# Kernel optimization log

Measured on AMD Instinct MI355X. Metric: run time of the kernel, lower is better.

The kernel has to match this reference:

```python
import jax, jax.numpy as jnp
import numpy as np

B, S, D, H = 2, 2048, 1024, 16
HD = D // H
EPS = 1e-5


def layer_norm(x, g, b):
    m = jnp.mean(x, axis=-1, keepdims=True)
    v = jnp.mean(jnp.square(x - m), axis=-1, keepdims=True)
    return (x - m) * jax.lax.rsqrt(v + EPS) * g + b


def setup_inputs() -> dict:
    key = jax.random.key(0)
    ks = jax.random.split(key, 16)
    s = 0.02
    x = jax.random.normal(ks[0], (B, S, D), dtype=jnp.float32)
    mask = jax.random.randint(ks[1], (1, 1, S, S), 0, 2, dtype=jnp.int32)
    return {
        "x": x,
        "mask": mask,
        "Wq": jax.random.normal(ks[2], (D, D), jnp.float32) * s,
        "Wk": jax.random.normal(ks[3], (D, D), jnp.float32) * s,
        "Wv": jax.random.normal(ks[4], (D, D), jnp.float32) * s,
        "Wo": jax.random.normal(ks[5], (D, D), jnp.float32) * s,
        "bo": jax.random.normal(ks[6], (D,), jnp.float32) * s,
        "ln1_g": jnp.ones((D,), jnp.float32),
        "ln1_b": jnp.zeros((D,), jnp.float32),
        "W1": jax.random.normal(ks[7], (D, 4 * D), jnp.float32) * s,
        "b1": jax.random.normal(ks[8], (4 * D,), jnp.float32) * s,
        "W2": jax.random.normal(ks[9], (4 * D, D), jnp.float32) * s,
        "b2": jax.random.normal(ks[10], (D,), jnp.float32) * s,
        "ln2_g": jnp.ones((D,), jnp.float32),
        "ln2_b": jnp.zeros((D,), jnp.float32),
    }


def reference(x, mask, Wq, Wk, Wv, Wo, bo, ln1_g, ln1_b, W1, b1, W2, b2, ln2_g, ln2_b):
    # --- multi-head attention (dropout = identity in eval) ---
    q = (x @ Wq).reshape(B, S, H, HD)
    k = (x @ Wk).reshape(B, S, H, HD)
    v = (x @ Wv).reshape(B, S, H, HD)
    scores = jnp.einsum("bshd,bthd->bhst", q, k) / jnp.sqrt(jnp.float32(HD))
    scores = jnp.where(mask == 1, jnp.float32(-1e9), scores)
    p = jax.nn.softmax(scores, axis=-1)
    o = jnp.einsum("bhst,bthd->bshd", p, v).reshape(B, S, D)
    attn_out = o @ Wo + bo
    # --- residual with norm on the branch (note: norm applied to attn output) ---
    x = x + layer_norm(attn_out, ln1_g, ln1_b)
    # --- FFN: gelu after fc1 AND after fc2 (as in source) ---
    h = jax.nn.gelu(x @ W1 + b1, approximate=False)
    h = jax.nn.gelu(h @ W2 + b2, approximate=False)
    x = x + layer_norm(h, ln2_g, ln2_b)
    return x
```

## Files before the change

### kernel.cpp

```cpp
#include <hip/hip_runtime.h>
#include <hip/hip_bf16.h>
#include <cstdint>

#define BB 2
#define SS 2048
#define DD 1024
#define HH 16
#define HDIM 64
#define MROWS (BB*SS)

typedef __bf16 bf16;
using bf16x8 = __bf16 __attribute__((ext_vector_type(8)));
using bf16x4 = __bf16 __attribute__((ext_vector_type(4)));
using bf16x2 = __bf16 __attribute__((ext_vector_type(2)));
using f32x4  = float __attribute__((ext_vector_type(4)));

__device__ __forceinline__ float gelu_exact(float x) {
    return 0.5f * x * (1.f + erff(x * 0.70710678118654752f));
}

__device__ __forceinline__ void stage16(const bf16* g, bf16* lds_chunk_base, int lane) {
#if __has_builtin(__builtin_amdgcn_global_load_lds)
    __builtin_amdgcn_global_load_lds((const __attribute__((address_space(1))) void*)g,
                                     (__attribute__((address_space(3))) void*)lds_chunk_base,
                                     16, 0, 0);
#else
    *(bf16x8*)(lds_chunk_base + lane * 8) = *(const bf16x8*)g;
#endif
}

__global__ __launch_bounds__(256) void prep_kernel(
    const float* __restrict__ x, bf16* __restrict__ x_b,
    const int* __restrict__ mask, unsigned long long* __restrict__ maskb,
    const float* __restrict__ Wq, const float* __restrict__ Wk,
    const float* __restrict__ Wv, const float* __restrict__ Wo,
    const float* __restrict__ W1, const float* __restrict__ W2,
    bf16* __restrict__ Wqkv_t, bf16* __restrict__ Wo_t,
    bf16* __restrict__ W1_t, bf16* __restrict__ W2_t) {
    const int bid = blockIdx.x;
    if (bid < 4096) {
        int i = bid * 256 + threadIdx.x;
        float4 v = ((const float4*)x)[i];
        bf16x4 o;
        o[0] = (bf16)v.x; o[1] = (bf16)v.y; o[2] = (bf16)v.z; o[3] = (bf16)v.w;
        *(bf16x4*)(x_b + (size_t)i * 4) = o;
        return;
    }
    if (bid < 20480) {
        int gid = (bid - 4096) * 256 + threadIdx.x;
        int mv = mask[gid];
        unsigned long long bal = __ballot(mv == 1);
        if ((threadIdx.x & 63) == 0) maskb[gid >> 6] = bal;
        return;
    }
    int t = bid - 20480;
    const float* W; bf16* Wt; int K, N, bx, by;
    if (t < 4096) {
        int wsel = t >> 10;
        int tt = t & 1023;
        W  = (wsel == 0) ? Wq : (wsel == 1) ? Wk : (wsel == 2) ? Wv : Wo;
        Wt = (wsel == 3) ? Wo_t : (Wqkv_t + (size_t)wsel * 1024 * 1024);
        K = 1024; N = 1024; bx = (tt & 31) * 32; by = (tt >> 5) * 32;
    } else if (t < 8192) {
        int tt = t - 4096;
        W = W1; Wt = W1_t; K = 1024; N = 4096;
        bx = (tt & 127) * 32; by = (tt >> 7) * 32;
    } else {
        int tt = t - 8192;
        W = W2; Wt = W2_t; K = 4096; N = 1024;
        bx = (tt & 31) * 32; by = (tt >> 5) * 32;
    }
    __shared__ float tile[32][33];
    int tx = threadIdx.x & 31;
    int ty = threadIdx.x >> 5;
#pragma unroll
    for (int j = 0; j < 4; ++j)
        tile[ty + j * 8][tx] = W[(size_t)(by + ty + j * 8) * N + bx + tx];
    __syncthreads();
#pragma unroll
    for (int j = 0; j < 4; ++j)
        Wt[(size_t)(bx + ty + j * 8) * K + by + tx] = (bf16)tile[tx][ty + j * 8];
}

template <int EPI>
__global__ __launch_bounds__(256, 3) void gemm_bt(const bf16* __restrict__ A,
                                                  const bf16* __restrict__ Bt,
                                                  void* __restrict__ C,
                                                  void* __restrict__ C2,
                                                  const float* __restrict__ bias,
                                                  int M, int N, int K, int ldk) {
    __shared__ __align__(16) bf16 As[128 * 64];
    __shared__ __align__(16) bf16 Bs[128 * 64];
    const int tid  = threadIdx.x;
    const int lane = tid & 63;
    const int wave = tid >> 6;
    const int l16  = lane & 15;
    const int quad = lane >> 4;
    const int wm = wave >> 1, wn = wave & 1;
    const int m0 = blockIdx.y * 128, n0 = blockIdx.x * 128;
    const int z  = blockIdx.z;
    A  += (size_t)z * K;
    Bt += (size_t)z * K;

    f32x4 acc[4][4];
#pragma unroll
    for (int i = 0; i < 4; ++i)
#pragma unroll
        for (int j = 0; j < 4; ++j) acc[i][j] = (f32x4){0.f, 0.f, 0.f, 0.f};

    const int nsteps = K >> 6;
    for (int kt = 0; kt < nsteps; ++kt) {
        const int kbase = kt << 6;
#pragma unroll
        for (int c = 0; c < 4; ++c) {
            int chunk = wave * 4 + c;
            int gi = chunk * 64 + lane;
            int m  = gi >> 3;
            int cp = gi & 7;
            int g  = cp ^ (m & 7);
            stage16(A  + (size_t)(m0 + m) * ldk + kbase + g * 8, As + chunk * 512, lane);
            stage16(Bt + (size_t)(n0 + m) * ldk + kbase + g * 8, Bs + chunk * 512, lane);
        }
        __syncthreads();
#pragma unroll
        for (int ks = 0; ks < 2; ++ks) {
            bf16x8 af[4], bfr[4];
#pragma unroll
            for (int i = 0; i < 4; ++i) {
                int m = wm * 64 + i * 16 + l16;
                int g = ks * 4 + quad;
                af[i]  = *(const bf16x8*)(As + m * 64 + ((g ^ (m & 7)) * 8));
                int n = wn * 64 + i * 16 + l16;
                bfr[i] = *(const bf16x8*)(Bs + n * 64 + ((g ^ (n & 7)) * 8));
            }
#pragma unroll
            for (int i = 0; i < 4; ++i)
#pragma unroll
                for (int j = 0; j < 4; ++j)
                    acc[i][j] = __builtin_amdgcn_mfma_f32_16x16x32_bf16(af[i], bfr[j], acc[i][j], 0, 0, 0);
        }
        __syncthreads();
    }

    float* Cz = (EPI == 4) ? (z ? (float*)C2 : (float*)C) : nullptr;
#pragma unroll
    for (int i = 0; i < 4; ++i) {
        int row = m0 + wm * 64 + i * 16 + quad * 4;
#pragma unroll
        for (int j = 0; j < 4; ++j) {
            int col = n0 + wn * 64 + j * 16 + l16;
            float bv = (EPI == 2) ? bias[col] : 0.f;
#pragma unroll
            for (int r = 0; r < 4; ++r) {
                float v = acc[i][j][r];
                if (EPI == 2) v = gelu_exact(v + bv);
                size_t idx = (size_t)(row + r) * N + col;
                if (EPI == 4) Cz[idx] = v;
                else          ((bf16*)C)[idx] = (bf16)v;
            }
        }
    }
}

__global__ __launch_bounds__(512, 4) void flash_attn(const bf16* __restrict__ qkv,
                                                     const unsigned long long* __restrict__ maskb,
                                                     bf16* __restrict__ o) {
    __shared__ __align__(16) bf16 Ks[128 * 64];
    __shared__ __align__(16) bf16 Vts[64 * 136];
    const int tid  = threadIdx.x;
    const int lane = tid & 63;
    const int wave = tid >> 6;
    const int l16  = lane & 15;
    const int quad = lane >> 4;
    const int bh = blockIdx.y;
    const int b = bh >> 4, h = bh & 15;
    const int q0 = blockIdx.x * 128;
    const size_t rowb = (size_t)b * SS;
    const float SCL = 0.18033688011112042f;

    const size_t qrow = (rowb + q0 + wave * 16 + l16) * 3072 + h * 64;
    bf16x8 qf[2];
    {
        bf16x8 q0r = *(const bf16x8*)(qkv + qrow + quad * 8);
        bf16x8 q1r = *(const bf16x8*)(qkv + qrow + 32 + quad * 8);
#pragma unroll
        for (int j = 0; j < 8; ++j) {
            qf[0][j] = (bf16)((float)q0r[j] * SCL);
            qf[1][j] = (bf16)((float)q1r[j] * SCL);
        }
    }

    f32x4 oacc[4];
#pragma unroll
    for (int d = 0; d < 4; ++d) oacc[d] = (f32x4){0.f, 0.f, 0.f, 0.f};
    f32x4 lacc = (f32x4){0.f, 0.f, 0.f, 0.f};
    const int mrow32 = (q0 + wave * 16 + l16) * 32;

    bf16x8 ones;
#pragma unroll
    for (int j = 0; j < 8; ++j) ones[j] = (bf16)1.0f;

    const int vt_tc = (lane >> 4) * 32 + ((lane >> 1) & 3) * 8 + ((lane >> 3) & 1) * 4 + 2 * (lane & 1);
    const int vd8 = wave * 8;

    int kst[2], ksg[2];
#pragma unroll
    for (int c = 0; c < 2; ++c) {
        int gi = (wave * 2 + c) * 64 + lane;
        kst[c] = gi >> 3;
        ksg[c] = (gi & 7) ^ (kst[c] & 7);
    }

    bf16x8 kreg[2], vreg[2];
    ulonglong2 mwreg;
#pragma unroll
    for (int c = 0; c < 2; ++c)
        kreg[c] = *(const bf16x8*)(qkv + (rowb + kst[c]) * 3072 + 1024 + h * 64 + ksg[c] * 8);
    {
        const bf16* vg = qkv + (rowb + 2 * lane) * 3072 + 2048 + h * 64 + vd8;
        vreg[0] = *(const bf16x8*)(vg);
        vreg[1] = *(const bf16x8*)(vg + 3072);
    }
    mwreg = *(const ulonglong2*)(maskb + mrow32);

    for (int kt = 0; kt < SS / 128; ++kt) {
        __syncthreads();
#pragma unroll
        for (int c = 0; c < 2; ++c)
            *(bf16x8*)(Ks + (wave * 2 + c) * 512 + lane * 8) = kreg[c];
#pragma unroll
        for (int j = 0; j < 8; ++j) {
            bf16x2 pr; pr[0] = vreg[0][j]; pr[1] = vreg[1][j];
            *(bf16x2*)(Vts + (vd8 + j) * 136 + vt_tc) = pr;
        }
        ulonglong2 mw = mwreg;
        __syncthreads();

        if (kt + 1 < SS / 128) {
            const int t0n = (kt + 1) * 128;
#pragma unroll
            for (int c = 0; c < 2; ++c)
                kreg[c] = *(const bf16x8*)(qkv + (rowb + t0n + kst[c]) * 3072 + 1024 + h * 64 + ksg[c] * 8);
            {
                const bf16* vg = qkv + (rowb + t0n + 2 * lane) * 3072 + 2048 + h * 64 + vd8;
                vreg[0] = *(const bf16x8*)(vg);
                vreg[1] = *(const bf16x8*)(vg + 3072);
            }
            mwreg = *(const ulonglong2*)(maskb + mrow32 + (kt + 1) * 2);
        }

        f32x4 st[8];
        __builtin_amdgcn_s_setprio(1);
#pragma unroll
        for (int tg = 0; tg < 8; ++tg) {
            int tl = tg * 16 + l16;
            bf16x8 a0 = *(const bf16x8*)(Ks + tl * 64 + ((quad       ^ (tl & 7)) * 8));
            bf16x8 a1 = *(const bf16x8*)(Ks + tl * 64 + (((4 + quad) ^ (tl & 7)) * 8));
            f32x4 s = (f32x4){0.f, 0.f, 0.f, 0.f};
            s = __builtin_amdgcn_mfma_f32_16x16x32_bf16(a0, qf[0], s, 0, 0, 0);
            s = __builtin_amdgcn_mfma_f32_16x16x32_bf16(a1, qf[1], s, 0, 0, 0);
            st[tg] = s;
        }
        __builtin_amdgcn_s_setprio(0);

        unsigned long long s0 = mw.x >> (quad * 4);
        unsigned long long s1 = mw.y >> (quad * 4);
        bf16x8 pva[4];
#pragma unroll
        for (int tg = 0; tg < 8; ++tg) {
            unsigned int bits = (unsigned int)(((tg < 4) ? s0 : s1) >> ((tg & 3) * 16));
#pragma unroll
            for (int r = 0; r < 4; ++r) {
                float p = __builtin_amdgcn_exp2f(st[tg][r]);
                p = ((bits >> r) & 1u) ? 0.f : p;
                pva[tg >> 1][(tg & 1) * 4 + r] = (bf16)p;
            }
        }

        __builtin_amdgcn_s_setprio(1);
#pragma unroll
        for (int kc = 0; kc < 4; ++kc) {
#pragma unroll
            for (int dg = 0; dg < 4; ++dg) {
                bf16x8 bfrag = *(const bf16x8*)(Vts + (dg * 16 + l16) * 136 + kc * 32 + quad * 8);
                oacc[dg] = __builtin_amdgcn_mfma_f32_16x16x32_bf16(pva[kc], bfrag, oacc[dg], 0, 0, 0);
            }
            lacc = __builtin_amdgcn_mfma_f32_16x16x32_bf16(pva[kc], ones, lacc, 0, 0, 0);
        }
        __builtin_amdgcn_s_setprio(0);
    }

#pragma unroll
    for (int r = 0; r < 4; ++r) {
        float inv_l = 1.f / lacc[r];
        bf16* orow = o + (rowb + q0 + wave * 16 + quad * 4 + r) * DD + h * 64;
#pragma unroll
        for (int dg = 0; dg < 4; ++dg)
            orow[dg * 16 + l16] = (bf16)(oacc[dg][r] * inv_l);
    }
}

template <bool GELU, bool WB16>
__global__ __launch_bounds__(256) void ln_fused(const float* __restrict__ resid,
                                                const float* __restrict__ p0,
                                                const float* __restrict__ p1,
                                                const float* __restrict__ bias,
                                                const float* __restrict__ g,
                                                const float* __restrict__ bb,
                                                float* __restrict__ outf,
                                                bf16* __restrict__ outb) {
    const int row = blockIdx.x;
    const int tid = threadIdx.x;
    const size_t base = (size_t)row * DD + tid * 4;
    float4 a0 = *(const float4*)(p0 + base);
    float4 a1 = *(const float4*)(p1 + base);
    float4 bz = *(const float4*)(bias + tid * 4);
    float ax = a0.x + a1.x + bz.x;
    float ay = a0.y + a1.y + bz.y;
    float az = a0.z + a1.z + bz.z;
    float aw = a0.w + a1.w + bz.w;
    if (GELU) { ax = gelu_exact(ax); ay = gelu_exact(ay); az = gelu_exact(az); aw = gelu_exact(aw); }
    float s1 = ax + ay + az + aw;
    float s2 = ax * ax + ay * ay + az * az + aw * aw;
#pragma unroll
    for (int off = 32; off; off >>= 1) {
        s1 += __shfl_xor(s1, off, 64);
        s2 += __shfl_xor(s2, off, 64);
    }
    __shared__ float red[8];
    if ((tid & 63) == 0) { red[(tid >> 6) * 2] = s1; red[(tid >> 6) * 2 + 1] = s2; }
    __syncthreads();
    s1 = red[0] + red[2] + red[4] + red[6];
    s2 = red[1] + red[3] + red[5] + red[7];
    float mean = s1 * (1.f / DD);
    float var  = s2 * (1.f / DD) - mean * mean;
    float rs = rsqrtf(var + 1e-5f);
    float4 gv = *(const float4*)(g + tid * 4);
    float4 bv = *(const float4*)(bb + tid * 4);
    float4 rv = *(const float4*)(resid + base);
    float y0 = rv.x + (ax - mean) * rs * gv.x + bv.x;
    float y1 = rv.y + (ay - mean) * rs * gv.y + bv.y;
    float y2 = rv.z + (az - mean) * rs * gv.z + bv.z;
    float y3 = rv.w + (aw - mean) * rs * gv.w + bv.w;
    float4 yo = make_float4(y0, y1, y2, y3);
    *(float4*)(outf + base) = yo;
    if (WB16) {
        bf16x4 ob;
        ob[0] = (bf16)y0; ob[1] = (bf16)y1; ob[2] = (bf16)y2; ob[3] = (bf16)y3;
        *(bf16x4*)(outb + base) = ob;
    }
}

extern "C" void kernel_launch(void* const* d_in, const int* in_sizes, int n_in,
                              void* d_out, int out_size, void* d_ws, size_t ws_size,
                              hipStream_t stream) {
    const float* x    = (const float*)d_in[0];
    const int*   mask = (const int*)d_in[1];
    const float* Wq   = (const float*)d_in[2];
    const float* Wk   = (const float*)d_in[3];
    const float* Wv   = (const float*)d_in[4];
    const float* Wo   = (const float*)d_in[5];
    const float* bo   = (const float*)d_in[6];
    const float* ln1g = (const float*)d_in[7];
    const float* ln1b = (const float*)d_in[8];
    const float* W1   = (const float*)d_in[9];
    const float* b1   = (const float*)d_in[10];
    const float* W2   = (const float*)d_in[11];
    const float* b2   = (const float*)d_in[12];
    const float* ln2g = (const float*)d_in[13];
    const float* ln2b = (const float*)d_in[14];

    char* w = (char*)d_ws;
    bf16* Wqkv_t = (bf16*)w; w += (size_t)3072 * 1024 * 2;
    bf16* Wo_t   = (bf16*)w; w += (size_t)1024 * 1024 * 2;
    bf16* W1_t   = (bf16*)w; w += (size_t)4096 * 1024 * 2;
    bf16* W2_t   = (bf16*)w; w += (size_t)1024 * 4096 * 2;
    bf16* x_b    = (bf16*)w; w += (size_t)MROWS * DD * 2;
    bf16* qkv    = (bf16*)w; w += (size_t)MROWS * 3072 * 2;
    float* R     = (float*)w; w += (size_t)MROWS * DD * 8;
    float* x1_f  = (float*)w; w += (size_t)MROWS * DD * 4;
    unsigned long long* maskb = (unsigned long long*)w; w += (size_t)SS * 32 * 8;
    bf16* o_b  = x_b;
    bf16* x1_b = x_b;
    float* op0 = R;
    float* op1 = R + (size_t)MROWS * DD;
    bf16*  h_b = (bf16*)R;
    float* fp0 = (float*)d_out;
    float* fp1 = (float*)qkv;

    prep_kernel<<<32768, 256, 0, stream>>>(x, x_b, mask, maskb,
                                           Wq, Wk, Wv, Wo, W1, W2,
                                           Wqkv_t, Wo_t, W1_t, W2_t);

    gemm_bt<0><<<dim3(24, 32, 1), 256, 0, stream>>>(x_b, Wqkv_t, qkv, nullptr, nullptr, MROWS, 3072, 1024, 1024);
    flash_attn<<<dim3(SS / 128, BB * HH), 512, 0, stream>>>(qkv, maskb, o_b);
    gemm_bt<4><<<dim3(8, 32, 2), 256, 0, stream>>>(o_b, Wo_t, op0, op1, nullptr, MROWS, 1024, 512, 1024);
    ln_fused<false, true><<<MROWS, 256, 0, stream>>>(x, op0, op1, bo, ln1g, ln1b, x1_f, x1_b);
    gemm_bt<2><<<dim3(32, 32, 1), 256, 0, stream>>>(x1_b, W1_t, h_b, nullptr, b1, MROWS, 4096, 1024, 1024);
    gemm_bt<4><<<dim3(8, 32, 2), 256, 0, stream>>>(h_b, W2_t, fp0, fp1, nullptr, MROWS, 1024, 2048, 4096);
    ln_fused<true, false><<<MROWS, 256, 0, stream>>>(x1_f, fp0, fp1, b2, ln2g, ln2b, (float*)d_out, nullptr);
}
```

Baseline: 377.2 us.

## Add 256x256-tile 8-wave GEMM and use it for the QKV, FC1 and FC2 projections

Adds a new GEMM kernel with 256x256 block tiles, 512 threads, double-buffered LDS staging and a four-phase interleaved MFMA schedule per K-tile. It replaces the 128-tile GEMM for the QKV and FC1 projections and for FC2, which now uses 4-way split-K. The final layernorm kernel is widened to sum four partial outputs, with the extra partial buffers placed in reused workspace regions. Larger tiles raise operand reuse and cut global traffic, but the QKV grid drops to 192 blocks, fewer than the CU count, and split-K adds more fp32 partial traffic.

```diff
diff --git a/kernel.cpp b/kernel.cpp
--- a/kernel.cpp
+++ b/kernel.cpp
@@ -162,6 +162,169 @@
     }
 }
 
+template <int EPI>
+__global__ __launch_bounds__(512, 2) void gemm256(const bf16* __restrict__ A,
+                                                  const bf16* __restrict__ Bt,
+                                                  void* __restrict__ C0, void* __restrict__ C1,
+                                                  void* __restrict__ C2v, void* __restrict__ C3,
+                                                  const float* __restrict__ bias,
+                                                  int M, int N, int K, int ldk) {
+    __shared__ __align__(16) bf16 As[2 * 256 * 64];
+    __shared__ __align__(16) bf16 Bs[2 * 256 * 64];
+    const int tid  = threadIdx.x;
+    const int lane = tid & 63;
+    const int wave = tid >> 6;
+    const int l16  = lane & 15;
+    const int quad = lane >> 4;
+    const int wm = wave >> 2;
+    const int wn = wave & 3;
+    const int m0 = blockIdx.y * 256, n0 = blockIdx.x * 256;
+    const int z  = blockIdx.z;
+    A  += (size_t)z * K;
+    Bt += (size_t)z * K;
+
+    const int rl = lane >> 3;
+    const int cpn = lane & 7;
+    const bf16* pA[4]; const bf16* pB[4];
+    int ldsoff[4];
+#pragma unroll
+    for (int c = 0; c < 4; ++c) {
+        int row = wave * 32 + c * 8 + rl;
+        int g = cpn ^ (row & 7);
+        pA[c] = A + (size_t)(m0 + row) * ldk + g * 8;
+        pB[c] = Bt + (size_t)(n0 + row) * ldk + g * 8;
+        ldsoff[c] = (wave * 4 + c) * 512;
+    }
+
+    f32x4 acc[8][4];
+#pragma unroll
+    for (int i = 0; i < 8; ++i)
+#pragma unroll
+        for (int j = 0; j < 4; ++j) acc[i][j] = (f32x4){0.f, 0.f, 0.f, 0.f};
+
+    const int nt = K >> 6;
+
+    auto stage_tile = [&](int t) {
+        const int kb = t << 6;
+        bf16* dstA = As + (t & 1) * 16384;
+        bf16* dstB = Bs + (t & 1) * 16384;
+#pragma unroll
+        for (int c = 0; c < 4; ++c) stage16(pA[c] + kb, dstA + ldsoff[c], lane);
+#pragma unroll
+        for (int c = 0; c < 4; ++c) stage16(pB[c] + kb, dstB + ldsoff[c], lane);
+    };
+
+    stage_tile(0);
+    stage_tile(1);
+    asm volatile("s_waitcnt vmcnt(8)" ::: "memory");
+    __builtin_amdgcn_s_barrier();
+
+    for (int t = 0; t < nt; ++t) {
+        const bf16* AsP = As + (t & 1) * 16384;
+        const bf16* BsP = Bs + (t & 1) * 16384;
+        bf16x8 af[4][2], b0[2][2], b1[2][2];
+
+#pragma unroll
+        for (int i = 0; i < 4; ++i) {
+            int row = wm * 128 + i * 16 + l16;
+#pragma unroll
+            for (int kk = 0; kk < 2; ++kk)
+                af[i][kk] = *(const bf16x8*)(AsP + row * 64 + (((kk * 4 + quad) ^ (row & 7)) * 8));
+        }
+#pragma unroll
+        for (int j = 0; j < 2; ++j) {
+            int row = wn * 64 + j * 16 + l16;
+#pragma unroll
+            for (int kk = 0; kk < 2; ++kk)
+                b0[j][kk] = *(const bf16x8*)(BsP + row * 64 + (((kk * 4 + quad) ^ (row & 7)) * 8));
+        }
+        __builtin_amdgcn_s_barrier();
+        __builtin_amdgcn_s_setprio(1);
+#pragma unroll
+        for (int i = 0; i < 4; ++i)
+#pragma unroll
+            for (int j = 0; j < 2; ++j)
+#pragma unroll
+                for (int kk = 0; kk < 2; ++kk)
+                    acc[i][j] = __builtin_amdgcn_mfma_f32_16x16x32_bf16(af[i][kk], b0[j][kk], acc[i][j], 0, 0, 0);
+        __builtin_amdgcn_s_setprio(0);
+        __builtin_amdgcn_s_barrier();
+
+#pragma unroll
+        for (int j = 0; j < 2; ++j) {
+            int row = wn * 64 + (j + 2) * 16 + l16;
+#pragma unroll
+            for (int kk = 0; kk < 2; ++kk)
+                b1[j][kk] = *(const bf16x8*)(BsP + row * 64 + (((kk * 4 + quad) ^ (row & 7)) * 8));
+        }
+        __builtin_amdgcn_s_barrier();
+        __builtin_amdgcn_s_setprio(1);
+#pragma unroll
+        for (int i = 0; i < 4; ++i)
+#pragma unroll
+            for (int j = 0; j < 2; ++j)
+#pragma unroll
+                for (int kk = 0; kk < 2; ++kk)
+                    acc[i][j + 2] = __builtin_amdgcn_mfma_f32_16x16x32_bf16(af[i][kk], b1[j][kk], acc[i][j + 2], 0, 0, 0);
+        __builtin_amdgcn_s_setprio(0);
+        __builtin_amdgcn_s_barrier();
+
+#pragma unroll
+        for (int i = 0; i < 4; ++i) {
+            int row = wm * 128 + 64 + i * 16 + l16;
+#pragma unroll
+            for (int kk = 0; kk < 2; ++kk)
+                af[i][kk] = *(const bf16x8*)(AsP + row * 64 + (((kk * 4 + quad) ^ (row & 7)) * 8));
+        }
+        __builtin_amdgcn_s_barrier();
+        __builtin_amdgcn_s_setprio(1);
+#pragma unroll
+        for (int i = 0; i < 4; ++i)
+#pragma unroll
+            for (int j = 0; j < 2; ++j)
+#pragma unroll
+                for (int kk = 0; kk < 2; ++kk)
+                    acc[i + 4][j + 2] = __builtin_amdgcn_mfma_f32_16x16x32_bf16(af[i][kk], b1[j][kk], acc[i + 4][j + 2], 0, 0, 0);
+        __builtin_amdgcn_s_setprio(0);
+        __builtin_amdgcn_s_barrier();
+
+        if (t + 2 < nt) stage_tile(t + 2);
+        __builtin_amdgcn_s_barrier();
+        __builtin_amdgcn_s_setprio(1);
+#pragma unroll
+        for (int i = 0; i < 4; ++i)
+#pragma unroll
+            for (int j = 0; j < 2; ++j)
+#pragma unroll
+                for (int kk = 0; kk < 2; ++kk)
+                    acc[i + 4][j] = __builtin_amdgcn_mfma_f32_16x16x32_bf16(af[i][kk], b0[j][kk], acc[i + 4][j], 0, 0, 0);
+        __builtin_amdgcn_s_setprio(0);
+        if (t + 2 < nt) { asm volatile("s_waitcnt vmcnt(8)" ::: "memory"); }
+        else            { asm volatile("s_waitcnt vmcnt(0)" ::: "memory"); }
+        __builtin_amdgcn_s_barrier();
+    }
+
+    float* Cz = nullptr;
+    if (EPI == 4) Cz = (z == 0) ? (float*)C0 : (z == 1) ? (float*)C1 : (z == 2) ? (float*)C2v : (float*)C3;
+#pragma unroll
+    for (int i = 0; i < 8; ++i) {
+        int row = m0 + wm * 128 + i * 16 + quad * 4;
+#pragma unroll
+        for (int j = 0; j < 4; ++j) {
+            int col = n0 + wn * 64 + j * 16 + l16;
+            float bv = (EPI == 2) ? bias[col] : 0.f;
+#pragma unroll
+            for (int r = 0; r < 4; ++r) {
+                float v = acc[i][j][r];
+                if (EPI == 2) v = gelu_exact(v + bv);
+                size_t idx = (size_t)(row + r) * N + col;
+                if (EPI == 4) Cz[idx] = v;
+                else          ((bf16*)C0)[idx] = (bf16)v;
+            }
+        }
+    }
+}
+
 __global__ __launch_bounds__(512, 4) void flash_attn(const bf16* __restrict__ qkv,
                                                      const unsigned long long* __restrict__ maskb,
                                                      bf16* __restrict__ o) {
@@ -300,10 +463,12 @@
     }
 }
 
-template <bool GELU, bool WB16>
+template <bool GELU, bool WB16, int NP>
 __global__ __launch_bounds__(256) void ln_fused(const float* __restrict__ resid,
                                                 const float* __restrict__ p0,
                                                 const float* __restrict__ p1,
+                                                const float* __restrict__ p2,
+                                                const float* __restrict__ p3,
                                                 const float* __restrict__ bias,
                                                 const float* __restrict__ g,
                                                 const float* __restrict__ bb,
@@ -319,6 +484,11 @@
     float ay = a0.y + a1.y + bz.y;
     float az = a0.z + a1.z + bz.z;
     float aw = a0.w + a1.w + bz.w;
+    if (NP == 4) {
+        float4 a2 = *(const float4*)(p2 + base);
+        float4 a3 = *(const float4*)(p3 + base);
+        ax += a2.x + a3.x; ay += a2.y + a3.y; az += a2.z + a3.z; aw += a2.w + a3.w;
+    }
     if (GELU) { ax = gelu_exact(ax); ay = gelu_exact(ay); az = gelu_exact(az); aw = gelu_exact(aw); }
     float s1 = ax + ay + az + aw;
     float s2 = ax * ax + ay * ay + az * az + aw * aw;
@@ -386,17 +556,19 @@
     float* op1 = R + (size_t)MROWS * DD;
     bf16*  h_b = (bf16*)R;
     float* fp0 = (float*)d_out;
-    float* fp1 = (float*)qkv;
+    float* fp1 = (float*)x_b;
+    float* fp2 = (float*)x_b + (size_t)4 * 1024 * 1024;
+    float* fp3 = (float*)d_ws;
 
     prep_kernel<<<32768, 256, 0, stream>>>(x, x_b, mask, maskb,
                                            Wq, Wk, Wv, Wo, W1, W2,
                                            Wqkv_t, Wo_t, W1_t, W2_t);
 
-    gemm_bt<0><<<dim3(24, 32, 1), 256, 0, stream>>>(x_b, Wqkv_t, qkv, nullptr, nullptr, MROWS, 3072, 1024, 1024);
+    gemm256<0><<<dim3(12, 16, 1), 512, 0, stream>>>(x_b, Wqkv_t, qkv, nullptr, nullptr, nullptr, nullptr, MROWS, 3072, 1024, 1024);
     flash_attn<<<dim3(SS / 128, BB * HH), 512, 0, stream>>>(qkv, maskb, o_b);
     gemm_bt<4><<<dim3(8, 32, 2), 256, 0, stream>>>(o_b, Wo_t, op0, op1, nullptr, MROWS, 1024, 512, 1024);
-    ln_fused<false, true><<<MROWS, 256, 0, stream>>>(x, op0, op1, bo, ln1g, ln1b, x1_f, x1_b);
-    gemm_bt<2><<<dim3(32, 32, 1), 256, 0, stream>>>(x1_b, W1_t, h_b, nullptr, b1, MROWS, 4096, 1024, 1024);
-    gemm_bt<4><<<dim3(8, 32, 2), 256, 0, stream>>>(h_b, W2_t, fp0, fp1, nullptr, MROWS, 1024, 2048, 4096);
-    ln_fused<true, false><<<MROWS, 256, 0, stream>>>(x1_f, fp0, fp1, b2, ln2g, ln2b, (float*)d_out, nullptr);
-}
+    ln_fused<false, true, 2><<<MROWS, 256, 0, stream>>>(x, op0, op1, nullptr, nullptr, bo, ln1g, ln1b, x1_f, x1_b);
+    gemm256<2><<<dim3(16, 16, 1), 512, 0, stream>>>(x1_b, W1_t, h_b, nullptr, nullptr, nullptr, b1, MROWS, 4096, 1024, 1024);
+    gemm256<4><<<dim3(4, 16, 4), 512, 0, stream>>>(h_b, W2_t, fp0, fp1, fp2, fp3, nullptr, MROWS, 1024, 1024, 4096);
+    ln_fused<true, false, 4><<<MROWS, 256, 0, stream>>>(x1_f, fp0, fp1, fp2, fp3, b2, ln2g, ln2b, (float*)d_out, nullptr);
+}
```

New measurement: 438.0 us. 1.16x slower.
